# Kernel optimization log

Measured on AMD Instinct MI355X. Metric: run time of the kernel, lower is better.

Reference implementation:

```python
import jax, jax.numpy as jnp
import numpy as np

VOCAB, EMBED, HIDDEN, FEAT = 193, 256, 512, 512
MAX_LEN = 15


def setup_inputs() -> dict:
    key = jax.random.key(0)
    ks = jax.random.split(key, 12)
    B = 8192
    s = 0.05  # small init scale for weights
    return {
        "img_feats": jax.random.normal(ks[0], (B, FEAT), jnp.float32),
        "text": jax.random.randint(ks[1], (B, MAX_LEN), 0, VOCAB, jnp.int64),
        "emb": jax.random.uniform(ks[2], (VOCAB, EMBED), jnp.float32, -0.1, 0.1),
        "W_proj": jax.random.normal(ks[3], (HIDDEN, FEAT), jnp.float32) * s,
        "b_proj": jnp.zeros((HIDDEN,), jnp.float32),
        "W_ih": jax.random.normal(ks[4], (3 * HIDDEN, EMBED), jnp.float32) * s,
        "W_hh": jax.random.normal(ks[5], (3 * HIDDEN, HIDDEN), jnp.float32) * s,
        "b_ih": jax.random.normal(ks[6], (3 * HIDDEN,), jnp.float32) * s,
        "b_hh": jax.random.normal(ks[7], (3 * HIDDEN,), jnp.float32) * s,
        "W_out": jax.random.uniform(ks[8], (VOCAB, HIDDEN), jnp.float32, -0.1, 0.1),
        "b_out": jnp.zeros((VOCAB,), jnp.float32),
    }


def reference(img_feats, text, emb, W_proj, b_proj, W_ih, W_hh, b_ih, b_hh, W_out, b_out):
    # h0 = project(img_feats)   [B, H]
    h0 = img_feats @ W_proj.T + b_proj
    # Teacher-forced decoder inputs: tokens text[:, 0..13] -> embeddings [T=14, B, E]
    xs = emb[text[:, : MAX_LEN - 1]].transpose(1, 0, 2)

    def gru_step(h, x):
        gi = x @ W_ih.T + b_ih   # [B, 3H]
        gh = h @ W_hh.T + b_hh   # [B, 3H]
        i_r, i_z, i_n = jnp.split(gi, 3, axis=-1)
        h_r, h_z, h_n = jnp.split(gh, 3, axis=-1)
        r = jax.nn.sigmoid(i_r + h_r)
        z = jax.nn.sigmoid(i_z + h_z)
        n = jnp.tanh(i_n + r * h_n)
        h_new = (1.0 - z) * n + z * h
        return h_new, h_new

    _, hs = jax.lax.scan(gru_step, h0, xs)  # hs: [T, B, H]
    preds = hs @ W_out.T + b_out            # [T, B, V]
    return preds.transpose(1, 0, 2)         # [B, T=14, V]
```

## Files before the change

kernel.cpp:

```cpp
#include <hip/hip_runtime.h>
#include <stdint.h>

using bf16x8 = __attribute__((ext_vector_type(8))) __bf16;
using f32x4  = __attribute__((ext_vector_type(4))) float;

#define AS1 __attribute__((address_space(1)))
#define AS3 __attribute__((address_space(3)))

constexpr size_t OFF_WHH   = 0;
constexpr size_t OFF_WPROJ = OFF_WHH   + (size_t)1536*512*2;
constexpr size_t OFF_WOUT  = OFF_WPROJ + (size_t)512*512*2;
constexpr size_t OFF_BHN   = OFF_WOUT  + (size_t)256*512*2;
constexpr size_t OFF_BPROJ = OFF_BHN   + 2048;
constexpr size_t OFF_BOUT  = OFF_BPROJ + 2048;
constexpr size_t OFF_EP    = OFF_BOUT  + 1024;
constexpr size_t OFF_HS    = OFF_EP    + (size_t)193*512*16;
constexpr size_t OFF_IMG   = OFF_HS    + (size_t)15*8192*512*2;
constexpr size_t WS_NEED   = OFF_IMG   + (size_t)8192*512*2;

constexpr size_t SLAB = (size_t)8192 * 512;

__device__ __forceinline__ short f2bf(float f) {
  union { float f; unsigned u; } v; v.f = f;
  unsigned u = v.u;
  u += 0x7FFFu + ((u >> 16) & 1u);
  return (short)(u >> 16);
}
__device__ __forceinline__ float bf2f(short s) {
  union { float f; unsigned u; } v; v.u = ((unsigned)(unsigned short)s) << 16;
  return v.f;
}
__device__ __forceinline__ float sigm(float x) { return 1.f / (1.f + __expf(-x)); }
__device__ __forceinline__ float tanh_fast(float x) {
  x = fminf(fmaxf(x, -15.f), 15.f);
  float e = __expf(-2.f * x);
  return (1.f - e) / (1.f + e);
}

template<int ROWS, int WAVES>
__device__ __forceinline__ void stage_tile(const short* __restrict__ src, size_t row0,
                                           int stride, int k0, char* lds, int tid) {
  const int w = tid >> 6;
  const int lane = tid & 63;
#pragma unroll
  for (int s = 0; s < ROWS / (8 * WAVES); ++s) {
    const int rowbase = s * (8 * WAVES) + w * 8;
    const int row = rowbase + (lane >> 3);
    const int colE = ((lane & 7) ^ (row & 7)) * 8;
    const short* g = src + (row0 + (size_t)row) * (size_t)stride + k0 + colE;
    __builtin_amdgcn_global_load_lds((const AS1 int*)g, (AS3 int*)(lds + rowbase * 128),
                                     16, 0, 0);
  }
}

__device__ __forceinline__ bf16x8 read_frag(const char* lds, int row, int ks, int lane) {
  const int kb = ks * 64 + ((lane >> 4) << 4);
  return *(const bf16x8*)(lds + row * 128 + (kb ^ ((row & 7) << 4)));
}

__global__ void prep_kernel(const float* __restrict__ W_proj, const float* __restrict__ b_proj,
                            const float* __restrict__ W_hh, const float* __restrict__ b_hh,
                            const float* __restrict__ W_out, const float* __restrict__ b_out,
                            short* __restrict__ whh, short* __restrict__ wproj,
                            short* __restrict__ wout,
                            float* __restrict__ bhn, float* __restrict__ bproj,
                            float* __restrict__ bout) {
  const int total = 1536*512 + 512*512 + 256*512 + 512 + 512 + 256;
  const int stride = gridDim.x * blockDim.x;
  for (int i = blockIdx.x * blockDim.x + threadIdx.x; i < total; i += stride) {
    int j = i;
    if (j < 1536*512) { whh[j] = f2bf(W_hh[j]); continue; }
    j -= 1536*512;
    if (j < 512*512) { wproj[j] = f2bf(W_proj[j]); continue; }
    j -= 512*512;
    if (j < 256*512) {
      int r = j / 512, c = j % 512;
      wout[j] = f2bf(r < 193 ? W_out[r*512 + c] : 0.f);
      continue;
    }
    j -= 256*512;
    if (j < 512) { bhn[j] = b_hh[1024 + j]; continue; }
    j -= 512;
    if (j < 512) { bproj[j] = b_proj[j]; continue; }
    j -= 512;
    bout[j] = (j < 193) ? b_out[j] : 0.f;
  }
}

__global__ void embproj_kernel(const float* __restrict__ emb, const float* __restrict__ W_ih,
                               const float* __restrict__ b_ih, const float* __restrict__ b_hh,
                               float4* __restrict__ ep4) {
  const int idx = blockIdx.x * blockDim.x + threadIdx.x;
  if (idx >= 193 * 512) return;
  const int v = idx >> 9, j = idx & 511;
  const float* er  = emb + (size_t)v * 256;
  const float* w_r = W_ih + (size_t)j * 256;
  const float* w_z = W_ih + (size_t)(512 + j) * 256;
  const float* w_n = W_ih + (size_t)(1024 + j) * 256;
  float sr = 0.f, sz = 0.f, sn = 0.f;
#pragma unroll 4
  for (int k = 0; k < 256; k += 4) {
    const float4 a = *(const float4*)(er + k);
    const float4 br = *(const float4*)(w_r + k);
    const float4 bz = *(const float4*)(w_z + k);
    const float4 bn = *(const float4*)(w_n + k);
    sr += a.x*br.x + a.y*br.y + a.z*br.z + a.w*br.w;
    sz += a.x*bz.x + a.y*bz.y + a.z*bz.z + a.w*bz.w;
    sn += a.x*bn.x + a.y*bn.y + a.z*bn.z + a.w*bn.w;
  }
  sr += b_ih[j] + b_hh[j];
  sz += b_ih[512 + j] + b_hh[512 + j];
  sn += b_ih[1024 + j];
  ep4[idx] = make_float4(sr, sz, sn, 0.f);
}

__global__ void imgcvt_kernel(const float* __restrict__ img, short* __restrict__ imgbf) {
  const int i = blockIdx.x * blockDim.x + threadIdx.x;
  const float4 v = *(const float4*)(img + (size_t)i * 4);
  short4 o; o.x = f2bf(v.x); o.y = f2bf(v.y); o.z = f2bf(v.z); o.w = f2bf(v.w);
  *(short4*)(imgbf + (size_t)i * 4) = o;
}

template<int MODE>
__global__ __launch_bounds__(256, 4)
void gemm_kernel(const short* __restrict__ A, const short* __restrict__ Bw,
                 const float* __restrict__ bias, float* __restrict__ out_f,
                 short* __restrict__ out_bf) {
  __shared__ __align__(16) char smem[40960];
  char* ldsA = smem;
  char* ldsB = smem + 8192;
  const int tid = threadIdx.x;
  const int lane = tid & 63;
  const int w = tid >> 6;
  const int wr = w >> 1, wc = w & 1;
  const unsigned m0 = blockIdx.x * 64;
  const int j0 = blockIdx.y * 256;

  f32x4 acc[2][8];
#pragma unroll
  for (int a = 0; a < 2; ++a)
#pragma unroll
    for (int b = 0; b < 8; ++b) acc[a][b] = f32x4{0.f, 0.f, 0.f, 0.f};

  for (int it = 0; it < 8; ++it) {
    const int k0 = it * 64;
    __syncthreads();
    if (MODE == 0) {
      stage_tile<64, 4>(A, m0, 512, k0, ldsA, tid);
    } else {
#pragma unroll
      for (int s = 0; s < 2; ++s) {
        const int rowbase = s * 32 + w * 8;
        const int row = rowbase + (lane >> 3);
        const unsigned m = m0 + row;
        const unsigned b = m / 14u, t = m - b * 14u;
        const int colE = ((lane & 7) ^ (row & 7)) * 8;
        const short* g = A + ((size_t)t * 8192 + b) * 512 + k0 + colE;
        __builtin_amdgcn_global_load_lds((const AS1 int*)g, (AS3 int*)(ldsA + rowbase * 128),
                                         16, 0, 0);
      }
    }
    stage_tile<256, 4>(Bw, (size_t)j0, 512, k0, ldsB, tid);
    __syncthreads();
#pragma unroll
    for (int ks = 0; ks < 2; ++ks) {
      bf16x8 af[2];
#pragma unroll
      for (int mi = 0; mi < 2; ++mi)
        af[mi] = read_frag(ldsA, wr*32 + mi*16 + (lane & 15), ks, lane);
#pragma unroll
      for (int ji = 0; ji < 8; ++ji) {
        bf16x8 bfm = read_frag(ldsB, wc*128 + ji*16 + (lane & 15), ks, lane);
#pragma unroll
        for (int mi = 0; mi < 2; ++mi)
          acc[mi][ji] = __builtin_amdgcn_mfma_f32_16x16x32_bf16(af[mi], bfm, acc[mi][ji], 0, 0, 0);
      }
    }
  }
#pragma unroll
  for (int ji = 0; ji < 8; ++ji) {
    const int j = j0 + wc*128 + ji*16 + (lane & 15);
    const float bj = bias[j];
#pragma unroll
    for (int mi = 0; mi < 2; ++mi) {
#pragma unroll
      for (int i = 0; i < 4; ++i) {
        const size_t m = m0 + wr*32 + mi*16 + ((lane >> 4) * 4) + i;
        const float v = acc[mi][ji][i] + bj;
        if (MODE == 0) {
          out_bf[m * 512 + j] = f2bf(v);
        } else {
          if (j < 193) out_f[m * 193 + j] = v;
        }
      }
    }
  }
}

__global__ __launch_bounds__(256, 2)
void gate_kernel(const short* __restrict__ Hbf, const short* __restrict__ whh,
                 const int* __restrict__ text, const int t,
                 const float4* __restrict__ ep4, const float* __restrict__ bhn,
                 short* __restrict__ hs_out) {
  __shared__ __align__(16) char smem[81920];
  char* ldsA0 = smem;
  char* ldsA1 = smem + 16384;
  char* ldsB0 = smem + 32768;
  char* ldsB1 = smem + 57344;
  const int tid = threadIdx.x;
  const int lane = tid & 63;
  const int w = tid >> 6;
  const int wr = w >> 1, wc = w & 1;
  const size_t m0 = (size_t)blockIdx.x * 128;
  const int j0 = blockIdx.y * 64;

  int toks[4][4];
#pragma unroll
  for (int mi = 0; mi < 4; ++mi)
#pragma unroll
    for (int i = 0; i < 4; ++i) {
      const size_t m = m0 + wr*64 + mi*16 + ((lane >> 4) * 4) + i;
      toks[mi][i] = text[m * 15 + t];
    }

  f32x4 acc_r[4][2], acc_z[4][2], acc_hn[4][2];
#pragma unroll
  for (int a = 0; a < 4; ++a)
#pragma unroll
    for (int b = 0; b < 2; ++b) {
      acc_r[a][b] = f32x4{0.f, 0.f, 0.f, 0.f};
      acc_z[a][b] = f32x4{0.f, 0.f, 0.f, 0.f};
      acc_hn[a][b] = f32x4{0.f, 0.f, 0.f, 0.f};
    }

  for (int it = 0; it < 4; ++it) {
    const int k0 = it * 128;
    __syncthreads();
    stage_tile<128, 4>(Hbf, m0, 512, k0, ldsA0, tid);
    stage_tile<128, 4>(Hbf, m0, 512, k0 + 64, ldsA1, tid);
#pragma unroll
    for (int g = 0; g < 3; ++g) {
      stage_tile<64, 4>(whh, (size_t)(g * 512 + j0), 512, k0,      ldsB0 + g * 8192, tid);
      stage_tile<64, 4>(whh, (size_t)(g * 512 + j0), 512, k0 + 64, ldsB1 + g * 8192, tid);
    }
    __syncthreads();
#pragma unroll
    for (int half = 0; half < 2; ++half) {
      const char* lA = half ? ldsA1 : ldsA0;
      const char* lB = half ? ldsB1 : ldsB0;
#pragma unroll
      for (int ks = 0; ks < 2; ++ks) {
        bf16x8 af[4];
#pragma unroll
        for (int mi = 0; mi < 4; ++mi)
          af[mi] = read_frag(lA, wr*64 + mi*16 + (lane & 15), ks, lane);
#pragma unroll
        for (int ji = 0; ji < 2; ++ji) {
          const int nb = wc*32 + ji*16 + (lane & 15);
          bf16x8 b_r = read_frag(lB,         nb, ks, lane);
          bf16x8 b_z = read_frag(lB + 8192,  nb, ks, lane);
          bf16x8 b_n = read_frag(lB + 16384, nb, ks, lane);
#pragma unroll
          for (int mi = 0; mi < 4; ++mi) {
            acc_r[mi][ji]  = __builtin_amdgcn_mfma_f32_16x16x32_bf16(af[mi], b_r, acc_r[mi][ji], 0, 0, 0);
            acc_z[mi][ji]  = __builtin_amdgcn_mfma_f32_16x16x32_bf16(af[mi], b_z, acc_z[mi][ji], 0, 0, 0);
            acc_hn[mi][ji] = __builtin_amdgcn_mfma_f32_16x16x32_bf16(af[mi], b_n, acc_hn[mi][ji], 0, 0, 0);
          }
        }
      }
    }
  }
#pragma unroll
  for (int ji = 0; ji < 2; ++ji) {
    const int j = j0 + wc*32 + ji*16 + (lane & 15);
    const float vbhn = bhn[j];
#pragma unroll
    for (int mi = 0; mi < 4; ++mi) {
#pragma unroll
      for (int i = 0; i < 4; ++i) {
        const size_t m = m0 + wr*64 + mi*16 + ((lane >> 4) * 4) + i;
        const float4 e = ep4[(size_t)toks[mi][i] * 512 + j];
        const float r = sigm(acc_r[mi][ji][i] + e.x);
        const float z = sigm(acc_z[mi][ji][i] + e.y);
        const float n = tanh_fast(e.z + r * (acc_hn[mi][ji][i] + vbhn));
        const float hold = bf2f(Hbf[m * 512 + j]);
        hs_out[m * 512 + j] = f2bf((1.f - z) * n + z * hold);
      }
    }
  }
}

extern "C" void kernel_launch(void* const* d_in, const int* in_sizes, int n_in,
                              void* d_out, int out_size, void* d_ws, size_t ws_size,
                              hipStream_t stream) {
  (void)in_sizes; (void)n_in; (void)out_size;
  if (ws_size < WS_NEED) return;

  const float* img    = (const float*)d_in[0];
  const int*   text   = (const int*)  d_in[1];
  const float* emb    = (const float*)d_in[2];
  const float* W_proj = (const float*)d_in[3];
  const float* b_proj = (const float*)d_in[4];
  const float* W_ih   = (const float*)d_in[5];
  const float* W_hh   = (const float*)d_in[6];
  const float* b_ih   = (const float*)d_in[7];
  const float* b_hh   = (const float*)d_in[8];
  const float* W_out  = (const float*)d_in[9];
  const float* b_out  = (const float*)d_in[10];
  float* out = (float*)d_out;
  char* ws = (char*)d_ws;

  short* whh   = (short*)(ws + OFF_WHH);
  short* wproj = (short*)(ws + OFF_WPROJ);
  short* wout  = (short*)(ws + OFF_WOUT);
  float* bhn   = (float*)(ws + OFF_BHN);
  float* bproj = (float*)(ws + OFF_BPROJ);
  float* bout  = (float*)(ws + OFF_BOUT);
  float4* ep4  = (float4*)(ws + OFF_EP);
  short* hs    = (short*)(ws + OFF_HS);
  short* imgbf = (short*)(ws + OFF_IMG);

  prep_kernel<<<512, 256, 0, stream>>>(W_proj, b_proj, W_hh, b_hh, W_out, b_out,
                                       whh, wproj, wout, bhn, bproj, bout);
  imgcvt_kernel<<<4096, 256, 0, stream>>>(img, imgbf);
  embproj_kernel<<<(193*512 + 255)/256, 256, 0, stream>>>(emb, W_ih, b_ih, b_hh, ep4);

  gemm_kernel<0><<<dim3(128, 2), 256, 0, stream>>>(imgbf, wproj, bproj, nullptr, hs);

  for (int t = 0; t < 14; ++t) {
    const short* Hb = hs + (size_t)t * SLAB;
    short* Ho       = hs + (size_t)(t + 1) * SLAB;
    gate_kernel<<<dim3(64, 8), 256, 0, stream>>>(Hb, whh, text, t, ep4, bhn, Ho);
  }

  gemm_kernel<1><<<dim3(1792, 1), 256, 0, stream>>>(hs + (size_t)8192 * 512, wout, bout,
                                                    out, nullptr);
}
```

Baseline: 413.7 us.

## Compute embedding-input projection with MFMA GEMM and remap gate blocks per XCD

Replaces the scalar fp32 embedding×W_ih projection kernel with a bf16 MFMA tiled GEMM. The weights and embeddings are converted to bf16 in the prep kernel, and the biases are pre-summed into a concatenated vector. The gate kernel launch is flattened to 1D and block indices are remapped so that consecutive M tiles land on the same XCD, aiming for better L2 reuse of hidden-state rows. The bf16 projection adds rounding error to the input gate terms.

```diff
diff --git a/kernel.cpp b/kernel.cpp
--- a/kernel.cpp
+++ b/kernel.cpp
@@ -10,10 +10,13 @@
 constexpr size_t OFF_WHH   = 0;
 constexpr size_t OFF_WPROJ = OFF_WHH   + (size_t)1536*512*2;
 constexpr size_t OFF_WOUT  = OFF_WPROJ + (size_t)512*512*2;
-constexpr size_t OFF_BHN   = OFF_WOUT  + (size_t)256*512*2;
+constexpr size_t OFF_WIH   = OFF_WOUT  + (size_t)256*512*2;
+constexpr size_t OFF_EMBBF = OFF_WIH   + (size_t)1536*256*2;
+constexpr size_t OFF_BHN   = OFF_EMBBF + (size_t)256*256*2;
 constexpr size_t OFF_BPROJ = OFF_BHN   + 2048;
 constexpr size_t OFF_BOUT  = OFF_BPROJ + 2048;
-constexpr size_t OFF_EP    = OFF_BOUT  + 1024;
+constexpr size_t OFF_BCAT  = OFF_BOUT  + 1024;
+constexpr size_t OFF_EP    = OFF_BCAT  + 1536*4;
 constexpr size_t OFF_HS    = OFF_EP    + (size_t)193*512*16;
 constexpr size_t OFF_IMG   = OFF_HS    + (size_t)15*8192*512*2;
 constexpr size_t WS_NEED   = OFF_IMG   + (size_t)8192*512*2;
@@ -60,12 +63,15 @@
 
 __global__ void prep_kernel(const float* __restrict__ W_proj, const float* __restrict__ b_proj,
                             const float* __restrict__ W_hh, const float* __restrict__ b_hh,
+                            const float* __restrict__ W_ih, const float* __restrict__ b_ih,
+                            const float* __restrict__ emb,
                             const float* __restrict__ W_out, const float* __restrict__ b_out,
                             short* __restrict__ whh, short* __restrict__ wproj,
-                            short* __restrict__ wout,
+                            short* __restrict__ wout, short* __restrict__ wih,
+                            short* __restrict__ embbf,
                             float* __restrict__ bhn, float* __restrict__ bproj,
-                            float* __restrict__ bout) {
-  const int total = 1536*512 + 512*512 + 256*512 + 512 + 512 + 256;
+                            float* __restrict__ bout, float* __restrict__ bcat) {
+  const int total = 1536*512 + 512*512 + 256*512 + 1536*256 + 256*256 + 512 + 512 + 256 + 1536;
   const int stride = gridDim.x * blockDim.x;
   for (int i = blockIdx.x * blockDim.x + threadIdx.x; i < total; i += stride) {
     int j = i;
@@ -79,39 +85,22 @@
       continue;
     }
     j -= 256*512;
+    if (j < 1536*256) { wih[j] = f2bf(W_ih[j]); continue; }
+    j -= 1536*256;
+    if (j < 256*256) {
+      int r = j >> 8, c = j & 255;
+      embbf[j] = f2bf(r < 193 ? emb[r*256 + c] : 0.f);
+      continue;
+    }
+    j -= 256*256;
     if (j < 512) { bhn[j] = b_hh[1024 + j]; continue; }
     j -= 512;
     if (j < 512) { bproj[j] = b_proj[j]; continue; }
     j -= 512;
-    bout[j] = (j < 193) ? b_out[j] : 0.f;
-  }
-}
-
-__global__ void embproj_kernel(const float* __restrict__ emb, const float* __restrict__ W_ih,
-                               const float* __restrict__ b_ih, const float* __restrict__ b_hh,
-                               float4* __restrict__ ep4) {
-  const int idx = blockIdx.x * blockDim.x + threadIdx.x;
-  if (idx >= 193 * 512) return;
-  const int v = idx >> 9, j = idx & 511;
-  const float* er  = emb + (size_t)v * 256;
-  const float* w_r = W_ih + (size_t)j * 256;
-  const float* w_z = W_ih + (size_t)(512 + j) * 256;
-  const float* w_n = W_ih + (size_t)(1024 + j) * 256;
-  float sr = 0.f, sz = 0.f, sn = 0.f;
-#pragma unroll 4
-  for (int k = 0; k < 256; k += 4) {
-    const float4 a = *(const float4*)(er + k);
-    const float4 br = *(const float4*)(w_r + k);
-    const float4 bz = *(const float4*)(w_z + k);
-    const float4 bn = *(const float4*)(w_n + k);
-    sr += a.x*br.x + a.y*br.y + a.z*br.z + a.w*br.w;
-    sz += a.x*bz.x + a.y*bz.y + a.z*bz.z + a.w*bz.w;
-    sn += a.x*bn.x + a.y*bn.y + a.z*bn.z + a.w*bn.w;
-  }
-  sr += b_ih[j] + b_hh[j];
-  sz += b_ih[512 + j] + b_hh[512 + j];
-  sn += b_ih[1024 + j];
-  ep4[idx] = make_float4(sr, sz, sn, 0.f);
+    if (j < 256) { bout[j] = (j < 193) ? b_out[j] : 0.f; continue; }
+    j -= 256;
+    bcat[j] = b_ih[j] + (j < 1024 ? b_hh[j] : 0.f);
+  }
 }
 
 __global__ void imgcvt_kernel(const float* __restrict__ img, short* __restrict__ imgbf) {
@@ -119,6 +108,62 @@
   const float4 v = *(const float4*)(img + (size_t)i * 4);
   short4 o; o.x = f2bf(v.x); o.y = f2bf(v.y); o.z = f2bf(v.z); o.w = f2bf(v.w);
   *(short4*)(imgbf + (size_t)i * 4) = o;
+}
+
+__global__ __launch_bounds__(256, 4)
+void embproj_mfma_kernel(const short* __restrict__ embbf, const short* __restrict__ wih,
+                         const float* __restrict__ bcat, float* __restrict__ ep) {
+  __shared__ __align__(16) char smem[40960];
+  char* ldsA = smem;
+  char* ldsB = smem + 8192;
+  const int tid = threadIdx.x;
+  const int lane = tid & 63;
+  const int w = tid >> 6;
+  const int wr = w >> 1, wc = w & 1;
+  const unsigned m0 = blockIdx.x * 64;
+  const int j0 = blockIdx.y * 256;
+
+  f32x4 acc[2][8];
+#pragma unroll
+  for (int a = 0; a < 2; ++a)
+#pragma unroll
+    for (int b = 0; b < 8; ++b) acc[a][b] = f32x4{0.f, 0.f, 0.f, 0.f};
+
+  for (int it = 0; it < 4; ++it) {
+    const int k0 = it * 64;
+    __syncthreads();
+    stage_tile<64, 4>(embbf, m0, 256, k0, ldsA, tid);
+    stage_tile<256, 4>(wih, (size_t)j0, 256, k0, ldsB, tid);
+    __syncthreads();
+#pragma unroll
+    for (int ks = 0; ks < 2; ++ks) {
+      bf16x8 af[2];
+#pragma unroll
+      for (int mi = 0; mi < 2; ++mi)
+        af[mi] = read_frag(ldsA, wr*32 + mi*16 + (lane & 15), ks, lane);
+#pragma unroll
+      for (int ji = 0; ji < 8; ++ji) {
+        bf16x8 bfm = read_frag(ldsB, wc*128 + ji*16 + (lane & 15), ks, lane);
+#pragma unroll
+        for (int mi = 0; mi < 2; ++mi)
+          acc[mi][ji] = __builtin_amdgcn_mfma_f32_16x16x32_bf16(af[mi], bfm, acc[mi][ji], 0, 0, 0);
+      }
+    }
+  }
+#pragma unroll
+  for (int ji = 0; ji < 8; ++ji) {
+    const int c = j0 + wc*128 + ji*16 + (lane & 15);
+    const int gate = c >> 9, jj = c & 511;
+    const float bc = bcat[c];
+#pragma unroll
+    for (int mi = 0; mi < 2; ++mi) {
+#pragma unroll
+      for (int i = 0; i < 4; ++i) {
+        const unsigned v = m0 + wr*32 + mi*16 + ((lane >> 4) * 4) + i;
+        if (v < 193) ep[((size_t)v * 512 + jj) * 4 + gate] = acc[mi][ji][i] + bc;
+      }
+    }
+  }
 }
 
 template<int MODE>
@@ -211,8 +256,11 @@
   const int lane = tid & 63;
   const int w = tid >> 6;
   const int wr = w >> 1, wc = w & 1;
-  const size_t m0 = (size_t)blockIdx.x * 128;
-  const int j0 = blockIdx.y * 64;
+  const unsigned raw = blockIdx.x;
+  const unsigned xcd = raw & 7, slot = raw >> 3;
+  const unsigned mt = xcd * 8 + (slot & 7), jt = slot >> 3;
+  const size_t m0 = (size_t)mt * 128;
+  const int j0 = jt * 64;
 
   int toks[4][4];
 #pragma unroll
@@ -313,24 +361,31 @@
   short* whh   = (short*)(ws + OFF_WHH);
   short* wproj = (short*)(ws + OFF_WPROJ);
   short* wout  = (short*)(ws + OFF_WOUT);
+  short* wih   = (short*)(ws + OFF_WIH);
+  short* embbf = (short*)(ws + OFF_EMBBF);
   float* bhn   = (float*)(ws + OFF_BHN);
   float* bproj = (float*)(ws + OFF_BPROJ);
   float* bout  = (float*)(ws + OFF_BOUT);
+  float* bcat  = (float*)(ws + OFF_BCAT);
+  float* epf   = (float*)(ws + OFF_EP);
   float4* ep4  = (float4*)(ws + OFF_EP);
   short* hs    = (short*)(ws + OFF_HS);
   short* imgbf = (short*)(ws + OFF_IMG);
 
-  prep_kernel<<<512, 256, 0, stream>>>(W_proj, b_proj, W_hh, b_hh, W_out, b_out,
-                                       whh, wproj, wout, bhn, bproj, bout);
+  prep_kernel<<<512, 256, 0, stream>>>(W_proj, b_proj, W_hh, b_hh, W_ih, b_ih, emb,
+                                       W_out, b_out,
+                                       whh, wproj, wout, wih, embbf,
+                                       bhn, bproj, bout, bcat);
   imgcvt_kernel<<<4096, 256, 0, stream>>>(img, imgbf);
-  embproj_kernel<<<(193*512 + 255)/256, 256, 0, stream>>>(emb, W_ih, b_ih, b_hh, ep4);
+
+  embproj_mfma_kernel<<<dim3(4, 6), 256, 0, stream>>>(embbf, wih, bcat, epf);
 
   gemm_kernel<0><<<dim3(128, 2), 256, 0, stream>>>(imgbf, wproj, bproj, nullptr, hs);
 
   for (int t = 0; t < 14; ++t) {
     const short* Hb = hs + (size_t)t * SLAB;
     short* Ho       = hs + (size_t)(t + 1) * SLAB;
-    gate_kernel<<<dim3(64, 8), 256, 0, stream>>>(Hb, whh, text, t, ep4, bhn, Ho);
+    gate_kernel<<<512, 256, 0, stream>>>(Hb, whh, text, t, ep4, bhn, Ho);
   }
 
   gemm_kernel<1><<<dim3(1792, 1), 256, 0, stream>>>(hs + (size_t)8192 * 512, wout, bout,
```

Result: faster. 378.5 us, median of 3 (-8.5%).
